# Performance work log

Hardware: AMD Instinct MI355X
Metric: run time of the kernel (lower is better)

The kernel has to match this reference:

```python
import jax, jax.numpy as jnp
import numpy as np

N_NODES = 50000
N_REL = 8
N_EDGES = 60000
F_IN = 128
UNITS = 128


def setup_inputs() -> dict:
    key = jax.random.key(0)
    ks = jax.random.split(key, 7)
    features = jax.random.normal(ks[0], (1, N_NODES, F_IN), dtype=jnp.float32)
    edge_src = jax.random.randint(ks[1], (N_REL, N_EDGES), 0, N_NODES, dtype=jnp.int32)
    edge_dst = jax.random.randint(ks[2], (N_REL, N_EDGES), 0, N_NODES, dtype=jnp.int32)
    edge_w = jax.random.uniform(ks[3], (N_REL, N_EDGES), dtype=jnp.float32)
    scale = 1.0 / np.sqrt(F_IN)
    self_kernel = jax.random.normal(ks[4], (F_IN, UNITS), dtype=jnp.float32) * scale
    rel_kernels = jax.random.normal(ks[5], (N_REL, F_IN, UNITS), dtype=jnp.float32) * scale
    bias = jnp.zeros((UNITS,), dtype=jnp.float32)
    return {"features": features, "edge_src": edge_src, "edge_dst": edge_dst,
            "edge_w": edge_w, "self_kernel": self_kernel,
            "rel_kernels": rel_kernels, "bias": bias}


def reference(features, edge_src, edge_dst, edge_w, self_kernel, rel_kernels, bias):
    # features: [1, N, F]; squeeze the batch dim like the original layer
    x = features[0]                                   # [N, F]
    out = x @ self_kernel                             # [N, U] self-loop term
    # per-relation feature transform: [R, N, U]
    hr = jnp.einsum('nf,rfu->rnu', x, rel_kernels)
    # sparse A_r @ hr via gather at src, weight, segment-sum into dst
    def per_rel(h, s, d, w):
        msg = h[s] * w[:, None]                       # [E, U]
        return jax.ops.segment_sum(msg, d, num_segments=N_NODES)
    agg = jax.vmap(per_rel)(hr, edge_src, edge_dst, edge_w)  # [R, N, U]
    out = out + agg.sum(axis=0) + bias
    out = jax.nn.relu(out)
    return out[None]                                  # [1, N, U]
```

## Files before the change

kernel.cpp:

```cpp
#include <hip/hip_runtime.h>
#include <hip/hip_bf16.h>

#define NN 50000
#define FF 128
#define UU 128
#define NREL 8
#define NE 60000
#define NKEY (NREL * NN)
#define NET (NREL * NE)

typedef __attribute__((ext_vector_type(8))) short bf16x8;
typedef __attribute__((ext_vector_type(4))) float f32x4;


__global__ __launch_bounds__(256) void prepbuild_kernel(
    const float* __restrict__ X, const float* __restrict__ Wself,
    const float* __restrict__ Wrel, const int* __restrict__ esrc,
    const int* __restrict__ edst, const float* __restrict__ ew,
    ushort* __restrict__ Xb, ushort* __restrict__ Wf,
    int* __restrict__ head, int4* __restrict__ rec)
{
    int i = blockIdx.x * 256 + threadIdx.x;
    if (i < NN * FF / 4) {
        float4 v = ((const float4*)X)[i];
        union { __hip_bfloat162 h[2]; uint2 u; } p;
        p.h[0] = __float22bfloat162_rn(make_float2(v.x, v.y));
        p.h[1] = __float22bfloat162_rn(make_float2(v.z, v.w));
        ((uint2*)Xb)[i] = p.u;
    }
    if (i < NET) {
        int key = (i / NE) * NN + edst[i];
        int prev = atomicExch(&head[key], i);
        rec[i] = make_int4(esrc[i], __float_as_int(ew[i]), prev, 0);
    }
    if (i < 9 * FF * UU) {
        int m = i >> 14, k = (i >> 7) & 127, col = i & 127;
        int c = col >> 4, al = col & 15;
        int s = k >> 5, ag = (k >> 3) & 3, j = k & 7;
        float v = (m == 0) ? Wself[i] : Wrel[i - FF * UU];
        __hip_bfloat16 h = __float2bfloat16(v);
        Wf[((m * 8 + c) * 4 + s) * 512 + (ag * 16 + al) * 8 + j] = *(ushort*)&h;
    }
}


#define AGG_L1R(i) int4 r##i = make_int4(0, 0, 0, 0); \
    if (e##i >= 0) r##i = rec[e##i];
#define AGG_L1X(i) uint x##i = 0u; \
    if (e##i >= 0) x##i = *(const uint*)(Xb + (size_t)r##i.x * FF + 2 * l);
#define AGG_L2R(i) int f##i = (e##i >= 0) ? r##i.z : -1; \
    int4 s##i = make_int4(0, 0, 0, 0); \
    if (f##i >= 0) s##i = rec[f##i];
#define AGG_L1A(i) if (e##i >= 0) { \
        float wgt = __int_as_float(r##i.y); \
        ax##i = fmaf(__uint_as_float(x##i << 16), wgt, ax##i); \
        ay##i = fmaf(__uint_as_float(x##i & 0xffff0000u), wgt, ay##i); }
#define AGG_L2X(i) uint y##i = 0u; \
    if (f##i >= 0) y##i = *(const uint*)(Xb + (size_t)s##i.x * FF + 2 * l);
#define AGG_L2A(i) if (f##i >= 0) { \
        float wgt = __int_as_float(s##i.y); \
        ax##i = fmaf(__uint_as_float(y##i << 16), wgt, ax##i); \
        ay##i = fmaf(__uint_as_float(y##i & 0xffff0000u), wgt, ay##i); \
        e##i = s##i.z; \
        if (e##i >= 0) r##i = rec[e##i]; \
    } else e##i = -1;

#define AGG_WALK(e, r, ax, ay)                                              \
    while (e >= 0) {                                                        \
        float w = __int_as_float(r.y);                                      \
        uint x = *(const uint*)(Xb + (size_t)r.x * FF + 2 * l);             \
        e = r.z;                                                            \
        if (e >= 0) r = rec[e];                                             \
        ax = fmaf(__uint_as_float(x << 16), w, ax);                         \
        ay = fmaf(__uint_as_float(x & 0xffff0000u), w, ay);                 \
    }

#define AGG_ST(i) { \
        __hip_bfloat162 hh = __float22bfloat162_rn(make_float2(ax##i, ay##i)); \
        *(uint*)(Zb + (size_t)(k0 + i) * FF + 2 * l) = *(uint*)&hh; }

__global__ __launch_bounds__(256) void agg_kernel(
    const ushort* __restrict__ Xb, const int* __restrict__ head,
    const int4* __restrict__ rec, ushort* __restrict__ Zb)
{
    const int k0 = ((blockIdx.x * 256 + threadIdx.x) >> 6) * 4;
    const int l = threadIdx.x & 63;

    float ax0 = 0.f, ay0 = 0.f, ax1 = 0.f, ay1 = 0.f;
    float ax2 = 0.f, ay2 = 0.f, ax3 = 0.f, ay3 = 0.f;

    const int4 hv = *(const int4*)&head[k0];
    int e0 = hv.x, e1 = hv.y, e2 = hv.z, e3 = hv.w;

    AGG_L1R(0) AGG_L1R(1) AGG_L1R(2) AGG_L1R(3)
    AGG_L1X(0) AGG_L1X(1) AGG_L1X(2) AGG_L1X(3)
    AGG_L2R(0) AGG_L2R(1) AGG_L2R(2) AGG_L2R(3)
    AGG_L1A(0) AGG_L1A(1) AGG_L1A(2) AGG_L1A(3)
    AGG_L2X(0) AGG_L2X(1) AGG_L2X(2) AGG_L2X(3)
    AGG_L2A(0) AGG_L2A(1) AGG_L2A(2) AGG_L2A(3)

    AGG_WALK(e0, r0, ax0, ay0)
    AGG_WALK(e1, r1, ax1, ay1)
    AGG_WALK(e2, r2, ax2, ay2)
    AGG_WALK(e3, r3, ax3, ay3)

    if (hv.x >= 0) AGG_ST(0)
    if (hv.y >= 0) AGG_ST(1)
    if (hv.z >= 0) AGG_ST(2)
    if (hv.w >= 0) AGG_ST(3)
}


__device__ __forceinline__ void gload_lds16(const uint4* g, uint4* l) {
    __builtin_amdgcn_global_load_lds(
        (const __attribute__((address_space(1))) void*)g,
        (__attribute__((address_space(3))) void*)l, 16, 0, 0);
}

#define LOAD_A(AF, P)                                                        \
    _Pragma("unroll")                                                        \
    for (int s = 0; s < 4; ++s)                                              \
        AF[s] = *(const bf16x8*)((P) + s * 32 + ag * 8);

#define LOAD_A_P(AF, P, NZ)                                                  \
    _Pragma("unroll")                                                        \
    for (int s = 0; s < 4; ++s) AF[s] = zfrag;                               \
    if (NZ) {                                                                \
        _Pragma("unroll")                                                    \
        for (int s = 0; s < 4; ++s)                                          \
            AF[s] = *(const bf16x8*)((P) + s * 32 + ag * 8);                 \
    }

#define MFMA_BURST(AF)                                                       \
    _Pragma("unroll")                                                        \
    for (int c = 0; c < 8; ++c) {                                            \
        _Pragma("unroll")                                                    \
        for (int s = 0; s < 4; ++s) {                                        \
            bf16x8 bfr = *(const bf16x8*)&bsh[(c * 4 + s) * 64 + l];         \
            acc[c] = __builtin_amdgcn_mfma_f32_16x16x32_bf16(                \
                AF[s], bfr, acc[c], 0, 0, 0);                                \
        }                                                                    \
    }

__global__ __launch_bounds__(256, 4) void gemm_kernel(
    const ushort* __restrict__ Xb, const ushort* __restrict__ Zb,
    const ushort* __restrict__ Wf, const int* __restrict__ head,
    const float* __restrict__ bias, float* __restrict__ out)
{
    __shared__ uint4 bsh[2048];
    const int t = threadIdx.x;
    const int wid = t >> 6;
    const int l = t & 63;
    const int gw0 = blockIdx.x * 4 + wid;
    const int gwid = (gw0 < NN / 16) ? gw0 : NN / 16 - 1;
    const int R0 = gwid * 16;
    const int al = l & 15;
    const int ag = l >> 4;
    const int arow = R0 + al;

    const uint4* Wf4 = (const uint4*)Wf;
    const bf16x8 zfrag = {0, 0, 0, 0, 0, 0, 0, 0};

    f32x4 acc[8];
    #pragma unroll
    for (int c = 0; c < 8; ++c) acc[c] = (f32x4){0.f, 0.f, 0.f, 0.f};

    uint nzmask = 0;
    #pragma unroll
    for (int mm = 0; mm < 8; ++mm)
        if (head[(size_t)mm * NN + arow] >= 0) nzmask |= (1u << mm);

    bf16x8 aA[4], aB[4];
    {
        const ushort* A0 = Xb + (size_t)arow * FF;
        LOAD_A(aA, A0)
    }

    #pragma unroll
    for (int m = 0; m < 9; ++m) {
        __syncthreads();
        {
            const uint4* Wm = Wf4 + m * 2048 + wid * 64 + l;
            uint4* lb = &bsh[wid * 64];
            #pragma unroll
            for (int k = 0; k < 8; ++k)
                gload_lds16(Wm + k * 256, lb + k * 256);
        }
        if (m < 8) {
            const ushort* An = Zb + ((size_t)m * NN + arow) * FF;
            const bool nz = (nzmask >> m) & 1;
            if ((m & 1) == 0) { LOAD_A_P(aB, An, nz) } else { LOAD_A_P(aA, An, nz) }
        }
        __syncthreads();
        if ((m & 1) == 0) { MFMA_BURST(aA) } else { MFMA_BURST(aB) }
    }

    #pragma unroll
    for (int c = 0; c < 8; ++c) {
        int col = c * 16 + al;
        float b = bias[col];
        #pragma unroll
        for (int q = 0; q < 4; ++q) {
            int row = R0 + ag * 4 + q;
            out[(size_t)row * UU + col] = fmaxf(acc[c][q] + b, 0.f);
        }
    }
}


extern "C" void kernel_launch(void* const* d_in, const int* in_sizes, int n_in,
                              void* d_out, int out_size, void* d_ws, size_t ws_size,
                              hipStream_t stream) {
    const float* X     = (const float*)d_in[0];
    const int*   esrc  = (const int*)d_in[1];
    const int*   edst  = (const int*)d_in[2];
    const float* ew    = (const float*)d_in[3];
    const float* Wself = (const float*)d_in[4];
    const float* Wrel  = (const float*)d_in[5];
    const float* bias  = (const float*)d_in[6];
    float* out = (float*)d_out;

    ushort* Zb   = (ushort*)d_ws;
    ushort* Xb   = Zb + (size_t)NKEY * FF;
    ushort* Wf   = Xb + (size_t)NN * FF;
    int*    head = (int*)(Wf + 9 * FF * UU);
    int4*   rec  = (int4*)(head + NKEY);

    hipMemsetAsync(head, 0xFF, NKEY * sizeof(int), stream);
    hipLaunchKernelGGL(prepbuild_kernel, dim3(NN * FF / 4 / 256), dim3(256), 0, stream,
                       X, Wself, Wrel, esrc, edst, ew, Xb, Wf, head, rec);
    hipLaunchKernelGGL(agg_kernel,  dim3(NKEY / 16), dim3(256), 0, stream,
                       Xb, head, rec, Zb);
    hipLaunchKernelGGL(gemm_kernel, dim3((NN / 16 + 3) / 4), dim3(256), 0, stream,
                       Xb, Zb, Wf, head, bias, out);
}
```

Measured before the change: 119.7 us.

## Triple-buffer weight half-tiles in LDS to overlap loads with MFMA

Splits each 128x128 weight tile into two half-tiles and streams them through a three-slot LDS ring. Each half-tile is prefetched two steps ahead, so the global-to-LDS loads overlap the MFMA bursts and each step needs only one barrier. The A-fragment load becomes unconditional, with the zero selected afterwards, which avoids a divergent branch but always reads the memory. LDS use grows from 32 KB to 48 KB per block and the occupancy hint drops from 4 to 3 blocks.

```diff
diff --git a/kernel.cpp b/kernel.cpp
--- a/kernel.cpp
+++ b/kernel.cpp
@@ -117,37 +117,43 @@
         (__attribute__((address_space(3))) void*)l, 16, 0, 0);
 }
 
+#define STAGE(q) { \
+        const uint4* Ws = Wf4 + ((q) >> 1) * 2048 + ((q) & 1) * 1024 + wid * 64 + l; \
+        uint4* lb = &bsh[((q) % 3) * 1024 + wid * 64]; \
+        _Pragma("unroll") \
+        for (int k = 0; k < 4; ++k) \
+            gload_lds16(Ws + k * 256, lb + k * 256); }
+
 #define LOAD_A(AF, P)                                                        \
     _Pragma("unroll")                                                        \
     for (int s = 0; s < 4; ++s)                                              \
         AF[s] = *(const bf16x8*)((P) + s * 32 + ag * 8);
 
-#define LOAD_A_P(AF, P, NZ)                                                  \
+#define LOAD_A_V(AF, P, NZ)                                                  \
     _Pragma("unroll")                                                        \
-    for (int s = 0; s < 4; ++s) AF[s] = zfrag;                               \
-    if (NZ) {                                                                \
-        _Pragma("unroll")                                                    \
-        for (int s = 0; s < 4; ++s)                                          \
-            AF[s] = *(const bf16x8*)((P) + s * 32 + ag * 8);                 \
-    }
-
-#define MFMA_BURST(AF)                                                       \
+    for (int s = 0; s < 4; ++s) {                                            \
+        bf16x8 tv = *(const bf16x8*)((P) + s * 32 + ag * 8);                 \
+        AF[s] = (NZ) ? tv : zfrag;                                           \
+    }
+
+#define HBURST(AF, p)                                                        \
     _Pragma("unroll")                                                        \
-    for (int c = 0; c < 8; ++c) {                                            \
+    for (int cl = 0; cl < 4; ++cl) {                                         \
         _Pragma("unroll")                                                    \
         for (int s = 0; s < 4; ++s) {                                        \
-            bf16x8 bfr = *(const bf16x8*)&bsh[(c * 4 + s) * 64 + l];         \
-            acc[c] = __builtin_amdgcn_mfma_f32_16x16x32_bf16(                \
-                AF[s], bfr, acc[c], 0, 0, 0);                                \
+            bf16x8 bfr = *(const bf16x8*)&bsh[((p) % 3) * 1024 +             \
+                                              (cl * 4 + s) * 64 + l];        \
+            acc[((p) & 1) * 4 + cl] = __builtin_amdgcn_mfma_f32_16x16x32_bf16( \
+                AF[s], bfr, acc[((p) & 1) * 4 + cl], 0, 0, 0);               \
         }                                                                    \
     }
 
-__global__ __launch_bounds__(256, 4) void gemm_kernel(
+__global__ __launch_bounds__(256, 3) void gemm_kernel(
     const ushort* __restrict__ Xb, const ushort* __restrict__ Zb,
     const ushort* __restrict__ Wf, const int* __restrict__ head,
     const float* __restrict__ bias, float* __restrict__ out)
 {
-    __shared__ uint4 bsh[2048];
+    __shared__ uint4 bsh[3 * 1024];
     const int t = threadIdx.x;
     const int wid = t >> 6;
     const int l = t & 63;
@@ -171,28 +177,23 @@
         if (head[(size_t)mm * NN + arow] >= 0) nzmask |= (1u << mm);
 
     bf16x8 aA[4], aB[4];
-    {
-        const ushort* A0 = Xb + (size_t)arow * FF;
-        LOAD_A(aA, A0)
-    }
-
-    #pragma unroll
-    for (int m = 0; m < 9; ++m) {
-        __syncthreads();
-        {
-            const uint4* Wm = Wf4 + m * 2048 + wid * 64 + l;
-            uint4* lb = &bsh[wid * 64];
-            #pragma unroll
-            for (int k = 0; k < 8; ++k)
-                gload_lds16(Wm + k * 256, lb + k * 256);
+    LOAD_A(aA, Xb + (size_t)arow * FF)
+    STAGE(0)
+    STAGE(1)
+    __syncthreads();
+
+    #pragma unroll
+    for (int p = 0; p < 18; ++p) {
+        if (p < 16) STAGE(p + 2)
+        if ((p & 1) == 0 && (p >> 1) < 8) {
+            const int mz = p >> 1;
+            const ushort* An = Zb + ((size_t)mz * NN + arow) * FF;
+            const bool nz = (nzmask >> mz) & 1;
+            if ((mz & 1) == 0) { LOAD_A_V(aB, An, nz) }
+            else               { LOAD_A_V(aA, An, nz) }
         }
-        if (m < 8) {
-            const ushort* An = Zb + ((size_t)m * NN + arow) * FF;
-            const bool nz = (nzmask >> m) & 1;
-            if ((m & 1) == 0) { LOAD_A_P(aB, An, nz) } else { LOAD_A_P(aA, An, nz) }
-        }
-        __syncthreads();
-        if ((m & 1) == 0) { MFMA_BURST(aA) } else { MFMA_BURST(aB) }
+        if (((p >> 1) & 1) == 0) { HBURST(aA, p) } else { HBURST(aB, p) }
+        if (p < 17) __syncthreads();
     }
 
     #pragma unroll
```

New measurement: 126.9 us. 1.06x slower.

## Double-buffer weight tiles in LDS to overlap staging with MFMA

Applied to the files above, without the earlier changes.

The GEMM kernel now keeps two LDS buffers for the per-relation weight tiles. It prefetches tile m+1 with global_load_lds while MFMAs consume tile m, which cuts the barriers per iteration from two to one. The cost is twice the LDS per block, so the launch-bounds occupancy hint drops from 4 to 2 blocks. That lower occupancy could reduce latency hiding for the A-fragment global loads.

```diff
diff --git a/kernel.cpp b/kernel.cpp
--- a/kernel.cpp
+++ b/kernel.cpp
@@ -117,6 +117,13 @@
         (__attribute__((address_space(3))) void*)l, 16, 0, 0);
 }
 
+#define STAGE(mm) { \
+        const uint4* Ws = Wf4 + (mm) * 2048 + wid * 64 + l; \
+        uint4* lb = &bsh[((mm) & 1) * 2048 + wid * 64]; \
+        _Pragma("unroll") \
+        for (int k = 0; k < 8; ++k) \
+            gload_lds16(Ws + k * 256, lb + k * 256); }
+
 #define LOAD_A(AF, P)                                                        \
     _Pragma("unroll")                                                        \
     for (int s = 0; s < 4; ++s)                                              \
@@ -131,23 +138,24 @@
             AF[s] = *(const bf16x8*)((P) + s * 32 + ag * 8);                 \
     }
 
-#define MFMA_BURST(AF)                                                       \
+#define MFMA_BURST(AF, mm)                                                   \
     _Pragma("unroll")                                                        \
     for (int c = 0; c < 8; ++c) {                                            \
         _Pragma("unroll")                                                    \
         for (int s = 0; s < 4; ++s) {                                        \
-            bf16x8 bfr = *(const bf16x8*)&bsh[(c * 4 + s) * 64 + l];         \
+            bf16x8 bfr = *(const bf16x8*)&bsh[((mm) & 1) * 2048 +            \
+                                              (c * 4 + s) * 64 + l];         \
             acc[c] = __builtin_amdgcn_mfma_f32_16x16x32_bf16(                \
                 AF[s], bfr, acc[c], 0, 0, 0);                                \
         }                                                                    \
     }
 
-__global__ __launch_bounds__(256, 4) void gemm_kernel(
+__global__ __launch_bounds__(256, 2) void gemm_kernel(
     const ushort* __restrict__ Xb, const ushort* __restrict__ Zb,
     const ushort* __restrict__ Wf, const int* __restrict__ head,
     const float* __restrict__ bias, float* __restrict__ out)
 {
-    __shared__ uint4 bsh[2048];
+    __shared__ uint4 bsh[2 * 2048];
     const int t = threadIdx.x;
     const int wid = t >> 6;
     const int l = t & 63;
@@ -171,28 +179,20 @@
         if (head[(size_t)mm * NN + arow] >= 0) nzmask |= (1u << mm);
 
     bf16x8 aA[4], aB[4];
-    {
-        const ushort* A0 = Xb + (size_t)arow * FF;
-        LOAD_A(aA, A0)
-    }
+    LOAD_A(aA, Xb + (size_t)arow * FF)
+    STAGE(0)
+    __syncthreads();
 
     #pragma unroll
     for (int m = 0; m < 9; ++m) {
-        __syncthreads();
-        {
-            const uint4* Wm = Wf4 + m * 2048 + wid * 64 + l;
-            uint4* lb = &bsh[wid * 64];
-            #pragma unroll
-            for (int k = 0; k < 8; ++k)
-                gload_lds16(Wm + k * 256, lb + k * 256);
-        }
         if (m < 8) {
+            STAGE(m + 1)
             const ushort* An = Zb + ((size_t)m * NN + arow) * FF;
             const bool nz = (nzmask >> m) & 1;
             if ((m & 1) == 0) { LOAD_A_P(aB, An, nz) } else { LOAD_A_P(aA, An, nz) }
         }
-        __syncthreads();
-        if ((m & 1) == 0) { MFMA_BURST(aA) } else { MFMA_BURST(aB) }
+        if ((m & 1) == 0) { MFMA_BURST(aA, m) } else { MFMA_BURST(aB, m) }
+        if (m < 8) __syncthreads();
     }
 
     #pragma unroll
```

Result: faster. 116.5 us (-2.7%).
